# Optimization experiments

Measured on AMD Instinct MI355X. Metric: run time of the kernel, lower is better.

## Reference

```python
import jax, jax.numpy as jnp
import numpy as np

B, S, D, H = 2, 4096, 768, 12
DH = D // H  # 64


def setup_inputs() -> dict:
    key = jax.random.key(0)
    k1, k2, k3, k4 = jax.random.split(key, 4)
    scale = 1.0 / np.sqrt(D)
    return {
        "X": jax.random.normal(k1, (B, S, D), dtype=jnp.float32),
        "W_q": jax.random.normal(k2, (D, D), dtype=jnp.float32) * scale,
        "W_k": jax.random.normal(k3, (D, D), dtype=jnp.float32) * scale,
        "W_v": jax.random.normal(k4, (D, D), dtype=jnp.float32) * scale,
    }


def reference(X, W_q, W_k, W_v):
    b, s, d = X.shape
    bias = -jnp.log(jnp.float32(s))  # sigmoid bias = -log(seq_len)
    # nn.Linear(d,d,bias=False): y = x @ W.T
    Q = (X @ W_q.T).reshape(b, s, H, DH).transpose(0, 2, 1, 3)  # [B,H,S,DH]
    K = (X @ W_k.T).reshape(b, s, H, DH).transpose(0, 2, 1, 3)
    V = (X @ W_v.T).reshape(b, s, H, DH).transpose(0, 2, 1, 3)
    scores = jnp.einsum("bhqd,bhkd->bhqk", Q, K) / jnp.sqrt(jnp.float32(DH))
    attn = jax.nn.sigmoid(scores + bias)  # no row normalization
    out = jnp.einsum("bhqk,bhkd->bhqd", attn, V)  # [B,H,S,DH]
    return out.transpose(0, 2, 1, 3).reshape(b, s, d)
```

## Files before the change

kernel.cpp:

```cpp
#include <hip/hip_runtime.h>

#define NHEAD 12
#define DHEAD 64
#define SEQ 4096
#define BATCH 2
#define DMODEL 768
#define M_TOTAL (BATCH * SEQ)

typedef __attribute__((ext_vector_type(8))) short bf16x8;
typedef __attribute__((ext_vector_type(4))) short s16x4;
typedef __attribute__((ext_vector_type(4))) float f32x4;
typedef unsigned short ushort_t;

__device__ __forceinline__ ushort_t f2bf(float f) {
  union { float f; unsigned u; } x; x.f = f;
  unsigned r = x.u + 0x7FFFu + ((x.u >> 16) & 1u);
  return (ushort_t)(r >> 16);
}

#define BM 128
#define BN 128
#define BK 32

__global__ __launch_bounds__(256) void qkv_gemm(
    const float* __restrict__ X, const float* __restrict__ Wq,
    const float* __restrict__ Wk, const float* __restrict__ Wv,
    ushort_t* __restrict__ qkv) {
  __shared__ __align__(16) ushort_t As[BM][BK];
  __shared__ __align__(16) ushort_t Bs[BN][BK];

  const float* W = (blockIdx.z == 0) ? Wq : ((blockIdx.z == 1) ? Wk : Wv);
  ushort_t* out = qkv + (size_t)blockIdx.z * (size_t)M_TOTAL * DMODEL;

  const int tid = threadIdx.x;
  const int lane = tid & 63, wave = tid >> 6;
  const int wr = wave >> 1, wc = wave & 1;
  const int m0 = blockIdx.x * BM, n0 = blockIdx.y * BN;
  const int l15 = lane & 15, l4 = lane >> 4;

  f32x4 acc[4][4] = {};

  for (int k0 = 0; k0 < DMODEL; k0 += BK) {
#pragma unroll
    for (int i = 0; i < 4; ++i) {
      int c = tid + i * 256;
      int row = c >> 3, col4 = c & 7;
      float4 a = *reinterpret_cast<const float4*>(
          &X[(size_t)(m0 + row) * DMODEL + k0 + col4 * 4]);
      float4 b = *reinterpret_cast<const float4*>(
          &W[(size_t)(n0 + row) * DMODEL + k0 + col4 * 4]);
      s16x4 ap, bp;
      ap[0] = (short)f2bf(a.x); ap[1] = (short)f2bf(a.y);
      ap[2] = (short)f2bf(a.z); ap[3] = (short)f2bf(a.w);
      bp[0] = (short)f2bf(b.x); bp[1] = (short)f2bf(b.y);
      bp[2] = (short)f2bf(b.z); bp[3] = (short)f2bf(b.w);
      *reinterpret_cast<s16x4*>(&As[row][col4 * 4]) = ap;
      *reinterpret_cast<s16x4*>(&Bs[row][col4 * 4]) = bp;
    }
    __syncthreads();

    bf16x8 af[4], bfr[4];
#pragma unroll
    for (int mi = 0; mi < 4; ++mi)
      af[mi] = *reinterpret_cast<const bf16x8*>(&As[wr * 64 + mi * 16 + l15][l4 * 8]);
#pragma unroll
    for (int ni = 0; ni < 4; ++ni)
      bfr[ni] = *reinterpret_cast<const bf16x8*>(&Bs[wc * 64 + ni * 16 + l15][l4 * 8]);
#pragma unroll
    for (int mi = 0; mi < 4; ++mi)
#pragma unroll
      for (int ni = 0; ni < 4; ++ni)
        acc[mi][ni] = __builtin_amdgcn_mfma_f32_16x16x32_bf16(
            af[mi], bfr[ni], acc[mi][ni], 0, 0, 0);
    __syncthreads();
  }

#pragma unroll
  for (int mi = 0; mi < 4; ++mi)
#pragma unroll
    for (int ni = 0; ni < 4; ++ni)
#pragma unroll
      for (int r = 0; r < 4; ++r) {
        int row = m0 + wr * 64 + mi * 16 + l4 * 4 + r;
        int col = n0 + wc * 64 + ni * 16 + l15;
        out[(size_t)row * DMODEL + col] = f2bf(acc[mi][ni][r]);
      }
}

#define BQ 128
#define KB 64

__global__ __launch_bounds__(256) void sig_attn(
    const ushort_t* __restrict__ qkv, float* __restrict__ out) {
  __shared__ __align__(16) ushort_t Ks[KB * DHEAD];
  __shared__ __align__(16) ushort_t Vt[DHEAD * KB];
  __shared__ __align__(16) ushort_t Ps[4][32 * KB];

  const int bh = blockIdx.y;
  const int b = bh / NHEAD, h = bh % NHEAD;
  const size_t SZ = (size_t)M_TOTAL * DMODEL;
  const ushort_t* Qg = qkv;
  const ushort_t* Kg = qkv + SZ;
  const ushort_t* Vg = qkv + 2 * SZ;

  const int tid = threadIdx.x, lane = tid & 63, wave = tid >> 6;
  const int l15 = lane & 15, l4 = lane >> 4;
  const int q0 = blockIdx.x * BQ + wave * 32;
  const size_t rowbase = (size_t)(b * SEQ) * DMODEL + h * DHEAD;

  bf16x8 qf[2][2];
#pragma unroll
  for (int mi = 0; mi < 2; ++mi)
#pragma unroll
    for (int ks = 0; ks < 2; ++ks)
      qf[mi][ks] = *reinterpret_cast<const bf16x8*>(
          &Qg[rowbase + (size_t)(q0 + mi * 16 + l15) * DMODEL + ks * 32 + l4 * 8]);

  f32x4 oacc[2][4] = {};
  const float c1 = -0.18033688f;
  const float c0 = 12.0f;

  for (int kt = 0; kt < SEQ; kt += KB) {
#pragma unroll
    for (int i = 0; i < 2; ++i) {
      int c = tid + i * 256;
      int row = c >> 3, c8 = c & 7;
      bf16x8 kv = *reinterpret_cast<const bf16x8*>(
          &Kg[rowbase + (size_t)(kt + row) * DMODEL + c8 * 8]);
      int dst = row * 64 + ((c8 * 8) ^ ((row & 7) << 3));
      *reinterpret_cast<bf16x8*>(&Ks[dst]) = kv;
      bf16x8 vv = *reinterpret_cast<const bf16x8*>(
          &Vg[rowbase + (size_t)(kt + row) * DMODEL + c8 * 8]);
#pragma unroll
      for (int j = 0; j < 8; ++j) {
        int dh = c8 * 8 + j;
        Vt[dh * 64 + (row ^ ((j ^ c8) << 3))] = (ushort_t)vv[j];
      }
    }
    __syncthreads();

    f32x4 s_acc[2][4] = {};
#pragma unroll
    for (int ks = 0; ks < 2; ++ks) {
      bf16x8 kf[4];
#pragma unroll
      for (int nt = 0; nt < 4; ++nt) {
        int row = nt * 16 + l15;
        kf[nt] = *reinterpret_cast<const bf16x8*>(
            &Ks[row * 64 + ((ks * 32 + l4 * 8) ^ ((row & 7) << 3))]);
      }
#pragma unroll
      for (int mi = 0; mi < 2; ++mi)
#pragma unroll
        for (int nt = 0; nt < 4; ++nt)
          s_acc[mi][nt] = __builtin_amdgcn_mfma_f32_16x16x32_bf16(
              qf[mi][ks], kf[nt], s_acc[mi][nt], 0, 0, 0);
    }

#pragma unroll
    for (int mi = 0; mi < 2; ++mi)
#pragma unroll
      for (int nt = 0; nt < 4; ++nt)
#pragma unroll
        for (int r = 0; r < 4; ++r) {
          float t = __builtin_fmaf(s_acc[mi][nt][r], c1, c0);
          float p = __builtin_amdgcn_rcpf(1.0f + __builtin_amdgcn_exp2f(t));
          int qrow = mi * 16 + l4 * 4 + r;
          int kcol = nt * 16 + l15;
          Ps[wave][qrow * 64 + (kcol ^ (((qrow & 7) ^ (qrow >> 3)) << 3))] = f2bf(p);
        }

#pragma unroll
    for (int ks = 0; ks < 2; ++ks) {
      bf16x8 pa[2];
#pragma unroll
      for (int mi = 0; mi < 2; ++mi) {
        int row = mi * 16 + l15;
        pa[mi] = *reinterpret_cast<const bf16x8*>(
            &Ps[wave][row * 64 +
                      ((ks * 32 + l4 * 8) ^ (((row & 7) ^ (row >> 3)) << 3))]);
      }
#pragma unroll
      for (int dt = 0; dt < 4; ++dt) {
        int row = dt * 16 + l15;
        bf16x8 vb = *reinterpret_cast<const bf16x8*>(
            &Vt[row * 64 +
                ((ks * 32 + l4 * 8) ^ (((row & 7) ^ (row >> 3)) << 3))]);
#pragma unroll
        for (int mi = 0; mi < 2; ++mi)
          oacc[mi][dt] = __builtin_amdgcn_mfma_f32_16x16x32_bf16(
              pa[mi], vb, oacc[mi][dt], 0, 0, 0);
      }
    }
    __syncthreads();
  }

#pragma unroll
  for (int mi = 0; mi < 2; ++mi)
#pragma unroll
    for (int dt = 0; dt < 4; ++dt)
#pragma unroll
      for (int r = 0; r < 4; ++r) {
        int s = q0 + mi * 16 + l4 * 4 + r;
        int dcol = dt * 16 + l15;
        out[(size_t)(b * SEQ + s) * DMODEL + h * DHEAD + dcol] = oacc[mi][dt][r];
      }
}

extern "C" void kernel_launch(void* const* d_in, const int* in_sizes, int n_in,
                              void* d_out, int out_size, void* d_ws, size_t ws_size,
                              hipStream_t stream) {
  const float* X  = (const float*)d_in[0];
  const float* Wq = (const float*)d_in[1];
  const float* Wk = (const float*)d_in[2];
  const float* Wv = (const float*)d_in[3];
  ushort_t* qkv = (ushort_t*)d_ws;

  dim3 gA(M_TOTAL / BM, DMODEL / BN, 3);
  qkv_gemm<<<gA, 256, 0, stream>>>(X, Wq, Wk, Wv, qkv);

  dim3 gB(SEQ / BQ, BATCH * NHEAD);
  sig_attn<<<gB, 256, 0, stream>>>(qkv, (float*)d_out);
}
```

Baseline: 352.4 us.

## Prefetch next GEMM K-tile into registers, pad LDS, use packed bf16 conversion

The QKV projection GEMM now loads the next K-slice of X and W into registers while the MFMAs of the current slice run, so global-load latency overlaps compute. The barrier placement moves to the top of the loop to fit this scheme. LDS rows are padded from 32 to 40 elements to reduce bank conflicts on fragment reads. The scalar software float-to-bf16 rounding is replaced with the hardware packed v_cvt_pk_bf16_f32 instruction in both staging and the epilogue. The changes add register pressure and rely on that instruction being available on the target.

```diff
diff --git a/kernel.cpp b/kernel.cpp
--- a/kernel.cpp
+++ b/kernel.cpp
@@ -10,6 +10,7 @@
 typedef __attribute__((ext_vector_type(8))) short bf16x8;
 typedef __attribute__((ext_vector_type(4))) short s16x4;
 typedef __attribute__((ext_vector_type(4))) float f32x4;
+typedef __attribute__((ext_vector_type(2))) unsigned u32x2;
 typedef unsigned short ushort_t;
 
 __device__ __forceinline__ ushort_t f2bf(float f) {
@@ -18,16 +19,23 @@
   return (ushort_t)(r >> 16);
 }
 
+__device__ __forceinline__ unsigned cvt_pk_bf16(float lo, float hi) {
+  unsigned r;
+  asm("v_cvt_pk_bf16_f32 %0, %1, %2" : "=v"(r) : "v"(lo), "v"(hi));
+  return r;
+}
+
 #define BM 128
 #define BN 128
 #define BK 32
+#define BKP 40
 
 __global__ __launch_bounds__(256) void qkv_gemm(
     const float* __restrict__ X, const float* __restrict__ Wq,
     const float* __restrict__ Wk, const float* __restrict__ Wv,
     ushort_t* __restrict__ qkv) {
-  __shared__ __align__(16) ushort_t As[BM][BK];
-  __shared__ __align__(16) ushort_t Bs[BN][BK];
+  __shared__ __align__(16) ushort_t As[BM][BKP];
+  __shared__ __align__(16) ushort_t Bs[BN][BKP];
 
   const float* W = (blockIdx.z == 0) ? Wq : ((blockIdx.z == 1) ? Wk : Wv);
   ushort_t* out = qkv + (size_t)blockIdx.z * (size_t)M_TOTAL * DMODEL;
@@ -40,24 +48,44 @@
 
   f32x4 acc[4][4] = {};
 
+  float4 ar[4], br[4];
+#pragma unroll
+  for (int i = 0; i < 4; ++i) {
+    int c = tid + i * 256;
+    int row = c >> 3, col4 = c & 7;
+    ar[i] = *reinterpret_cast<const float4*>(
+        &X[(size_t)(m0 + row) * DMODEL + col4 * 4]);
+    br[i] = *reinterpret_cast<const float4*>(
+        &W[(size_t)(n0 + row) * DMODEL + col4 * 4]);
+  }
+
   for (int k0 = 0; k0 < DMODEL; k0 += BK) {
+    __syncthreads();
 #pragma unroll
     for (int i = 0; i < 4; ++i) {
       int c = tid + i * 256;
       int row = c >> 3, col4 = c & 7;
-      float4 a = *reinterpret_cast<const float4*>(
-          &X[(size_t)(m0 + row) * DMODEL + k0 + col4 * 4]);
-      float4 b = *reinterpret_cast<const float4*>(
-          &W[(size_t)(n0 + row) * DMODEL + k0 + col4 * 4]);
-      s16x4 ap, bp;
-      ap[0] = (short)f2bf(a.x); ap[1] = (short)f2bf(a.y);
-      ap[2] = (short)f2bf(a.z); ap[3] = (short)f2bf(a.w);
-      bp[0] = (short)f2bf(b.x); bp[1] = (short)f2bf(b.y);
-      bp[2] = (short)f2bf(b.z); bp[3] = (short)f2bf(b.w);
-      *reinterpret_cast<s16x4*>(&As[row][col4 * 4]) = ap;
-      *reinterpret_cast<s16x4*>(&Bs[row][col4 * 4]) = bp;
-    }
-    __syncthreads();
+      u32x2 ap, bp;
+      ap[0] = cvt_pk_bf16(ar[i].x, ar[i].y);
+      ap[1] = cvt_pk_bf16(ar[i].z, ar[i].w);
+      bp[0] = cvt_pk_bf16(br[i].x, br[i].y);
+      bp[1] = cvt_pk_bf16(br[i].z, br[i].w);
+      *reinterpret_cast<u32x2*>(&As[row][col4 * 4]) = ap;
+      *reinterpret_cast<u32x2*>(&Bs[row][col4 * 4]) = bp;
+    }
+    __syncthreads();
+
+    if (k0 + BK < DMODEL) {
+#pragma unroll
+      for (int i = 0; i < 4; ++i) {
+        int c = tid + i * 256;
+        int row = c >> 3, col4 = c & 7;
+        ar[i] = *reinterpret_cast<const float4*>(
+            &X[(size_t)(m0 + row) * DMODEL + k0 + BK + col4 * 4]);
+        br[i] = *reinterpret_cast<const float4*>(
+            &W[(size_t)(n0 + row) * DMODEL + k0 + BK + col4 * 4]);
+      }
+    }
 
     bf16x8 af[4], bfr[4];
 #pragma unroll
@@ -72,7 +100,6 @@
       for (int ni = 0; ni < 4; ++ni)
         acc[mi][ni] = __builtin_amdgcn_mfma_f32_16x16x32_bf16(
             af[mi], bfr[ni], acc[mi][ni], 0, 0, 0);
-    __syncthreads();
   }
 
 #pragma unroll
@@ -80,10 +107,12 @@
 #pragma unroll
     for (int ni = 0; ni < 4; ++ni)
 #pragma unroll
-      for (int r = 0; r < 4; ++r) {
+      for (int r = 0; r < 4; r += 2) {
+        unsigned u = cvt_pk_bf16(acc[mi][ni][r], acc[mi][ni][r + 1]);
         int row = m0 + wr * 64 + mi * 16 + l4 * 4 + r;
         int col = n0 + wc * 64 + ni * 16 + l15;
-        out[(size_t)row * DMODEL + col] = f2bf(acc[mi][ni][r]);
+        out[(size_t)row * DMODEL + col] = (ushort_t)(u & 0xffffu);
+        out[(size_t)(row + 1) * DMODEL + col] = (ushort_t)(u >> 16);
       }
 }
 
```

Result: faster. 331.7 us (-5.9%).
